# Optimization experiments

Hardware: AMD Instinct MI355X
Metric: run time of the kernel (lower is better)

The kernel has to match this reference:

```python
import math
import jax, jax.numpy as jnp
import numpy as np

H = 1024
NH = 16
HD = H // NH
FF = 4096


def gelu_erf(x):
    return x * 0.5 * (1.0 + jax.lax.erf(x / jnp.sqrt(jnp.float32(2.0))))


def layernorm(x, gamma, beta, eps=1e-12):
    mean = x.mean(axis=-1, keepdims=True)
    var = ((x - mean) ** 2).mean(axis=-1, keepdims=True)
    return gamma * (x - mean) / jnp.sqrt(var + eps) + beta


def setup_inputs() -> dict:
    key = jax.random.key(0)
    ks = jax.random.split(key, 12)
    B, S = 2, 2048
    sc = 0.02
    return {
        "x": jax.random.normal(ks[0], (B, S, H), jnp.float32),
        "attention_mask": jnp.ones((B, S), jnp.int32),
        "Wq": jax.random.normal(ks[1], (H, H), jnp.float32) * sc,
        "bq": jnp.zeros((H,), jnp.float32),
        "Wk": jax.random.normal(ks[2], (H, H), jnp.float32) * sc,
        "bk": jnp.zeros((H,), jnp.float32),
        "Wv": jax.random.normal(ks[3], (H, H), jnp.float32) * sc,
        "bv": jnp.zeros((H,), jnp.float32),
        "Wo": jax.random.normal(ks[4], (H, H), jnp.float32) * sc,
        "bo": jnp.zeros((H,), jnp.float32),
        "ln1_g": jnp.ones((H,), jnp.float32),
        "ln1_b": jnp.zeros((H,), jnp.float32),
        "W1": jax.random.normal(ks[5], (H, FF), jnp.float32) * sc,
        "b1": jnp.zeros((FF,), jnp.float32),
        "W2": jax.random.normal(ks[6], (FF, H), jnp.float32) * sc,
        "b2": jnp.zeros((H,), jnp.float32),
        "ln2_g": jnp.ones((H,), jnp.float32),
        "ln2_b": jnp.zeros((H,), jnp.float32),
    }


def reference(x, attention_mask, Wq, bq, Wk, bk, Wv, bv, Wo, bo,
              ln1_g, ln1_b, W1, b1, W2, b2, ln2_g, ln2_b):
    B, S, _ = x.shape
    # QKV projections, split heads -> [B, NH, S, HD]
    def split(t):
        return t.reshape(B, S, NH, HD).transpose(0, 2, 1, 3)
    q = split(x @ Wq + bq)
    k = split(x @ Wk + bk)
    v = split(x @ Wv + bv)
    # scores [B, NH, S, S]
    s = jnp.einsum("bhqd,bhkd->bhqk", q, k) / math.sqrt(HD)
    mask = (attention_mask == 1)[:, None, None, :]  # [B,1,1,S]
    s = jnp.where(mask, s, -jnp.inf)
    p = jax.nn.softmax(s, axis=-1)
    a = jnp.einsum("bhqk,bhkd->bhqd", p, v)
    a = a.transpose(0, 2, 1, 3).reshape(B, S, H)  # merge heads
    a = a @ Wo + bo
    a = layernorm(a, ln1_g, ln1_b)  # NOTE: no residual in source
    m = gelu_erf(a @ W1 + b1) @ W2 + b2
    return layernorm(m, ln2_g, ln2_b)
```

## Files before the change

### kernel.cpp

```cpp
#include <hip/hip_runtime.h>
#include <hip/hip_bf16.h>
#include <math.h>

typedef __bf16 bf16;
typedef __attribute__((ext_vector_type(8))) __bf16 bf16x8;
typedef __attribute__((ext_vector_type(4))) __bf16 bf16x4;
typedef __attribute__((ext_vector_type(4))) float f32x4;

#define HDIM 1024
#define NHEAD 16
#define HD 64
#define FFDIM 4096
#define BATCH 2
#define SEQ 2048
#define M_TOK 4096
#define PSTRIDE ((size_t)M_TOK * HDIM)

static __device__ __forceinline__ void async_load16(const bf16* g, bf16* l) {
  __builtin_amdgcn_global_load_lds(
      (const __attribute__((address_space(1))) void*)g,
      (__attribute__((address_space(3))) void*)l, 16, 0, 0);
}

__global__ __launch_bounds__(256)
void prep_kernel(const float* __restrict__ x,
                 const float* __restrict__ Wq, const float* __restrict__ Wk,
                 const float* __restrict__ Wv, const float* __restrict__ Wo,
                 const float* __restrict__ W1, const float* __restrict__ W2,
                 bf16* __restrict__ Xb, bf16* __restrict__ QKVT,
                 bf16* __restrict__ W1T, bf16* __restrict__ W2T)
{
  const int z = blockIdx.z;
  const int t = threadIdx.x;
  if (z == 12) {
    const size_t base = ((size_t)(blockIdx.y * 32 + blockIdx.x)) * 4096;
#pragma unroll
    for (int j = 0; j < 4; ++j) {
      const size_t i = base + j * 1024 + t * 4;
      f32x4 v = *(const f32x4*)(x + i);
      bf16x4 o;
#pragma unroll
      for (int k = 0; k < 4; ++k) o[k] = (bf16)v[k];
      *(bf16x4*)(Xb + i) = o;
    }
    return;
  }
  const float* ps; bf16* pd; int sld, dld;
  if (z < 4) {
    ps = (z == 0) ? Wq : (z == 1) ? Wk : (z == 2) ? Wv : Wo;
    pd = QKVT + (size_t)z * HDIM * HDIM; sld = 1024; dld = 1024;
  } else if (z < 8) {
    const int c = z - 4;
    ps = W1 + c * 1024; sld = 4096;
    pd = W1T + (size_t)c * 1024 * 1024; dld = 1024;
  } else {
    const int c = z - 8;
    ps = W2 + (size_t)c * 1024 * 1024; sld = 1024;
    pd = W2T + c * 1024; dld = 4096;
  }
  __shared__ float tile[32][33];
  const int tx = t & 31, ty = t >> 5;
  const int c0 = blockIdx.x * 32, r0 = blockIdx.y * 32;
#pragma unroll
  for (int i = 0; i < 32; i += 8)
    tile[ty + i][tx] = ps[(size_t)(r0 + ty + i) * sld + c0 + tx];
  __syncthreads();
#pragma unroll
  for (int i = 0; i < 32; i += 8)
    pd[(size_t)(c0 + ty + i) * dld + r0 + tx] = (bf16)tile[tx][ty + i];
}

template<int EPI>
__global__ __launch_bounds__(256)
void gemm_bt(const bf16* __restrict__ A, const bf16* __restrict__ Bt,
             const float* __restrict__ b0, const float* __restrict__ b1p,
             const float* __restrict__ b2p, void* __restrict__ Cout,
             int M, int N, int ldk, int kchunk)
{
  __shared__ __align__(16) bf16 As[128 * 64];
  __shared__ __align__(16) bf16 Bs[128 * 64];
  const int t = threadIdx.x;
  const int wave = t >> 6, lane = t & 63;
  const int lm = lane & 15, qd = lane >> 4;
  const int wm = (wave >> 1) * 64, wn = (wave & 1) * 64;
  const int bm = blockIdx.y * 128, bn = blockIdx.x * 128;
  const int kbeg = blockIdx.z * kchunk;

  f32x4 acc[4][4] = {};
  const int srow = t >> 3;
  const int schk = t & 7;

  for (int k0 = kbeg; k0 < kbeg + kchunk; k0 += 64) {
#pragma unroll
    for (int r = 0; r < 4; ++r) {
      const int row = r * 32 + srow;
      const int chunk = schk ^ (row & 7);
      async_load16(A + (size_t)(bm + row) * ldk + (k0 + chunk * 8),
                   (bf16*)((char*)As + r * 4096 + t * 16));
    }
#pragma unroll
    for (int r = 0; r < 4; ++r) {
      const int row = r * 32 + srow;
      const int chunk = schk ^ (row & 7);
      async_load16(Bt + (size_t)(bn + row) * ldk + (k0 + chunk * 8),
                   (bf16*)((char*)Bs + r * 4096 + t * 16));
    }
    __syncthreads();
#pragma unroll
    for (int ks = 0; ks < 2; ++ks) {
      bf16x8 av[4], bv[4];
#pragma unroll
      for (int mt = 0; mt < 4; ++mt) {
        const int row = wm + mt * 16 + lm;
        const int chunk = (ks * 4 + qd) ^ (row & 7);
        av[mt] = *(const bf16x8*)(As + row * 64 + chunk * 8);
      }
#pragma unroll
      for (int nt = 0; nt < 4; ++nt) {
        const int row = wn + nt * 16 + lm;
        const int chunk = (ks * 4 + qd) ^ (row & 7);
        bv[nt] = *(const bf16x8*)(Bs + row * 64 + chunk * 8);
      }
#pragma unroll
      for (int mt = 0; mt < 4; ++mt)
#pragma unroll
        for (int nt = 0; nt < 4; ++nt)
          acc[mt][nt] = __builtin_amdgcn_mfma_f32_16x16x32_bf16(av[mt], bv[nt], acc[mt][nt], 0, 0, 0);
    }
    __syncthreads();
  }

#pragma unroll
  for (int nt = 0; nt < 4; ++nt) {
    const int col = bn + wn + nt * 16 + lm;
    float bs = 0.f;
    if (EPI == 2) bs = b0[col];
    if (EPI == 3) {
      const int sect = col >> 10, c = col & 1023;
      bs = (sect == 0) ? b0[c] : (sect == 1) ? b1p[c] : b2p[c];
    }
#pragma unroll
    for (int mt = 0; mt < 4; ++mt) {
#pragma unroll
      for (int r = 0; r < 4; ++r) {
        const int row = bm + wm + mt * 16 + qd * 4 + r;
        float v = acc[mt][nt][r] + bs;
        if (EPI == 1) {
          ((float*)Cout + (size_t)blockIdx.z * M * N)[(size_t)row * N + col] = v;
        } else if (EPI == 2) {
          const float z = v * 0.70710678118f;
          const float az = fabsf(z);
          const float tt = __builtin_amdgcn_rcpf(fmaf(az, 0.3275911f, 1.0f));
          const float poly = tt * fmaf(tt, fmaf(tt, fmaf(tt, fmaf(tt, 1.061405429f,
                             -1.453152027f), 1.421413741f), -0.284496736f), 0.254829592f);
          const float e = __builtin_amdgcn_exp2f(az * az * -1.4426950408889634f);
          float erfv = 1.0f - poly * e;
          erfv = (z < 0.f) ? -erfv : erfv;
          const float g = 0.5f * v * (1.0f + erfv);
          ((bf16*)Cout)[(size_t)row * N + col] = (bf16)g;
        } else {
          bf16* base = (bf16*)Cout;
          const int sect = col >> 10, c = col & 1023;
          if (sect < 2) {
            base[(size_t)sect * M_TOK * HDIM + (size_t)row * HDIM + c] = (bf16)v;
          } else {
            const int hh = c >> 6, dd = c & 63;
            const int bb = row >> 11, ss = row & 2047;
            base[(size_t)2 * M_TOK * HDIM +
                 (size_t)((bb * NHEAD + hh) * HD + dd) * SEQ + ss] = (bf16)v;
          }
        }
      }
    }
  }
}

__global__ __launch_bounds__(256)
void attn_kernel(const bf16* __restrict__ Q, const bf16* __restrict__ Kg,
                 const bf16* __restrict__ Vt, const int* __restrict__ mask,
                 bf16* __restrict__ Aout)
{
  __shared__ __align__(16) bf16 Ks[64 * 64];
  __shared__ __align__(16) bf16 Vs[64 * 64];
  __shared__ __align__(16) bf16 Ps[4][16 * 64];
  __shared__ float madd[64];

  const int t = threadIdx.x;
  const int wave = t >> 6, lane = t & 63;
  const int lm = lane & 15, qd = lane >> 4;
  const int bh = blockIdx.y;
  const int b = bh >> 4, h = bh & 15;
  const int q0 = blockIdx.x * 64;
  const int qg = q0 + wave * 16 + lm;
  bf16* Psw = Ps[wave];

  bf16x8 qf[2];
#pragma unroll
  for (int ks = 0; ks < 2; ++ks)
    qf[ks] = *(const bf16x8*)(Q + (size_t)(b * SEQ + qg) * HDIM + h * HD + ks * 32 + qd * 8);

  float l_lane = 0.f;
  f32x4 oacc[4] = {};

  const int srow = t >> 3, schk = t & 7;
  const float C = 0.1803368801f;

  for (int kv0 = 0; kv0 < SEQ; kv0 += 64) {
#pragma unroll
    for (int r = 0; r < 2; ++r) {
      const int row = r * 32 + srow;
      const int g = schk ^ (row & 7);
      async_load16(Kg + (size_t)(b * SEQ + kv0 + row) * HDIM + h * HD + g * 8,
                   (bf16*)((char*)Ks + r * 4096 + t * 16));
      async_load16(Vt + (size_t)(bh * HD + row) * SEQ + kv0 + g * 8,
                   (bf16*)((char*)Vs + r * 4096 + t * 16));
    }
    if (t < 64) madd[t] = (mask[b * SEQ + kv0 + t] == 1) ? 0.f : -1.0e30f;
    __syncthreads();

    f32x4 sacc[4] = {};
#pragma unroll
    for (int ks = 0; ks < 2; ++ks) {
#pragma unroll
      for (int nt = 0; nt < 4; ++nt) {
        const int row = nt * 16 + lm;
        const int c = (ks * 4 + qd) ^ (row & 7);
        bf16x8 kf = *(const bf16x8*)(Ks + row * 64 + c * 8);
        sacc[nt] = __builtin_amdgcn_mfma_f32_16x16x32_bf16(kf, qf[ks], sacc[nt], 0, 0, 0);
      }
    }

#pragma unroll
    for (int nt = 0; nt < 4; ++nt) {
      f32x4 ma = *(const f32x4*)(madd + nt * 16 + qd * 4);
      bf16x4 pk;
#pragma unroll
      for (int r = 0; r < 4; ++r) {
        const float pv = __builtin_amdgcn_exp2f(fmaf(sacc[nt][r], C, ma[r]));
        l_lane += pv;
        pk[r] = (bf16)pv;
      }
      *(bf16x4*)((char*)Psw + lm * 128 +
                 (((nt * 2 + (qd >> 1)) ^ (lm & 7)) * 16) + (qd & 1) * 8) = pk;
    }

#pragma unroll
    for (int ks = 0; ks < 2; ++ks) {
      bf16x8 pf = *(const bf16x8*)((char*)Psw + lm * 128 + (((ks * 4 + qd) ^ (lm & 7)) * 16));
#pragma unroll
      for (int nt = 0; nt < 4; ++nt) {
        const int row = nt * 16 + lm;
        const int c = (ks * 4 + qd) ^ (row & 7);
        bf16x8 vf = *(const bf16x8*)(Vs + row * 64 + c * 8);
        oacc[nt] = __builtin_amdgcn_mfma_f32_16x16x32_bf16(vf, pf, oacc[nt], 0, 0, 0);
      }
    }
    __syncthreads();
  }

  float l = l_lane;
  l += __shfl_xor(l, 16, 64);
  l += __shfl_xor(l, 32, 64);
  const float inv = 1.0f / l;

#pragma unroll
  for (int nt = 0; nt < 4; ++nt) {
    bf16x4 ok;
#pragma unroll
    for (int r = 0; r < 4; ++r) ok[r] = (bf16)(oacc[nt][r] * inv);
    *(bf16x4*)((char*)Psw + lm * 128 +
               (((nt * 2 + (qd >> 1)) ^ (lm & 7)) * 16) + (qd & 1) * 8) = ok;
  }
#pragma unroll
  for (int rr = 0; rr < 2; ++rr) {
    const int ql = rr * 8 + (lane >> 3);
    const int cl = lane & 7;
    bf16x8 v = *(const bf16x8*)((char*)Psw + ql * 128 + ((cl ^ (ql & 7)) * 16));
    *(bf16x8*)(Aout + (size_t)(b * SEQ + q0 + wave * 16 + ql) * HDIM + h * HD + cl * 8) = v;
  }
}

template<int NP, int OUT_BF16>
__global__ __launch_bounds__(256)
void ln_sum(const float* __restrict__ p, const float* __restrict__ bias,
            const float* __restrict__ gamma, const float* __restrict__ beta,
            void* __restrict__ out)
{
  const int row = blockIdx.x;
  const int t = threadIdx.x;
  f32x4 v = *(const f32x4*)(p + (size_t)row * HDIM + t * 4);
#pragma unroll
  for (int np = 1; np < NP; ++np) {
    f32x4 u = *(const f32x4*)(p + np * PSTRIDE + (size_t)row * HDIM + t * 4);
#pragma unroll
    for (int j = 0; j < 4; ++j) v[j] += u[j];
  }
  f32x4 bv0 = *(const f32x4*)(bias + t * 4);
#pragma unroll
  for (int j = 0; j < 4; ++j) v[j] += bv0[j];

  float s = v[0] + v[1] + v[2] + v[3];
  float s2 = v[0] * v[0] + v[1] * v[1] + v[2] * v[2] + v[3] * v[3];
#pragma unroll
  for (int d = 1; d < 64; d <<= 1) { s += __shfl_xor(s, d, 64); s2 += __shfl_xor(s2, d, 64); }
  __shared__ float ss[4], ss2[4];
  const int wave = t >> 6, lane = t & 63;
  if (lane == 0) { ss[wave] = s; ss2[wave] = s2; }
  __syncthreads();
  s = ss[0] + ss[1] + ss[2] + ss[3];
  s2 = ss2[0] + ss2[1] + ss2[2] + ss2[3];
  const float mean = s * (1.0f / HDIM);
  const float var = s2 * (1.0f / HDIM) - mean * mean;
  const float rstd = rsqrtf(var + 1e-12f);
  f32x4 gv = *(const f32x4*)(gamma + t * 4);
  f32x4 bv = *(const f32x4*)(beta + t * 4);
  f32x4 y;
#pragma unroll
  for (int j = 0; j < 4; ++j) y[j] = gv[j] * (v[j] - mean) * rstd + bv[j];
  if (OUT_BF16) {
    bf16x4 o;
#pragma unroll
    for (int j = 0; j < 4; ++j) o[j] = (bf16)y[j];
    *(bf16x4*)((bf16*)out + (size_t)row * HDIM + t * 4) = o;
  } else {
    *(f32x4*)((float*)out + (size_t)row * HDIM + t * 4) = y;
  }
}

extern "C" void kernel_launch(void* const* d_in, const int* in_sizes, int n_in,
                              void* d_out, int out_size, void* d_ws, size_t ws_size,
                              hipStream_t stream)
{
  const float* x    = (const float*)d_in[0];
  const int*   am   = (const int*)d_in[1];
  const float* Wq   = (const float*)d_in[2];
  const float* bq   = (const float*)d_in[3];
  const float* Wk   = (const float*)d_in[4];
  const float* bk   = (const float*)d_in[5];
  const float* Wv   = (const float*)d_in[6];
  const float* bv   = (const float*)d_in[7];
  const float* Wo   = (const float*)d_in[8];
  const float* bo   = (const float*)d_in[9];
  const float* ln1g = (const float*)d_in[10];
  const float* ln1b = (const float*)d_in[11];
  const float* W1   = (const float*)d_in[12];
  const float* b1   = (const float*)d_in[13];
  const float* W2   = (const float*)d_in[14];
  const float* b2   = (const float*)d_in[15];
  const float* ln2g = (const float*)d_in[16];
  const float* ln2b = (const float*)d_in[17];

  char* ws = (char*)d_ws;
  const size_t MB = 1ull << 20;
  bf16*  W1T  = (bf16*)(ws + 0 * MB);
  bf16*  W2T  = (bf16*)(ws + 8 * MB);
  bf16*  Xb   = (bf16*)(ws + 16 * MB);
  bf16*  QKVT = (bf16*)(ws + 24 * MB);
  bf16*  WoT  = QKVT + (size_t)3 * HDIM * HDIM;
  bf16*  Qb   = (bf16*)(ws + 33 * MB);
  bf16*  Kb   = (bf16*)(ws + 41 * MB);
  bf16*  Vtb  = (bf16*)(ws + 49 * MB);
  bf16*  Ab   = (bf16*)(ws + 16 * MB);
  float* Pw   = (float*)(ws + 33 * MB);
  bf16*  L1   = (bf16*)(ws + 65 * MB);
  bf16*  F1   = (bf16*)(ws + 16 * MB);
  float* Pf   = (float*)(ws + 48 * MB);

  prep_kernel<<<dim3(32, 32, 13), 256, 0, stream>>>(x, Wq, Wk, Wv, Wo, W1, W2,
                                                    Xb, QKVT, W1T, W2T);

  gemm_bt<3><<<dim3(3072 / 128, M_TOK / 128, 1), 256, 0, stream>>>(
      Xb, QKVT, bq, bk, bv, Qb, M_TOK, 3072, HDIM, HDIM);

  attn_kernel<<<dim3(SEQ / 64, BATCH * NHEAD), 256, 0, stream>>>(Qb, Kb, Vtb, am, Ab);

  gemm_bt<1><<<dim3(HDIM / 128, M_TOK / 128, 2), 256, 0, stream>>>(
      Ab, WoT, nullptr, nullptr, nullptr, Pw, M_TOK, HDIM, HDIM, 512);
  ln_sum<2, 1><<<M_TOK, 256, 0, stream>>>(Pw, bo, ln1g, ln1b, L1);

  gemm_bt<2><<<dim3(FFDIM / 128, M_TOK / 128, 1), 256, 0, stream>>>(
      L1, W1T, b1, nullptr, nullptr, F1, M_TOK, FFDIM, HDIM, HDIM);

  if (ws_size >= 113 * MB) {
    gemm_bt<1><<<dim3(HDIM / 128, M_TOK / 128, 4), 256, 0, stream>>>(
        F1, W2T, nullptr, nullptr, nullptr, Pf, M_TOK, HDIM, FFDIM, 1024);
    ln_sum<4, 0><<<M_TOK, 256, 0, stream>>>(Pf, b2, ln2g, ln2b, (float*)d_out);
  } else {
    gemm_bt<1><<<dim3(HDIM / 128, M_TOK / 128, 2), 256, 0, stream>>>(
        F1, W2T, nullptr, nullptr, nullptr, Pf, M_TOK, HDIM, FFDIM, 2048);
    ln_sum<2, 0><<<M_TOK, 256, 0, stream>>>(Pf, b2, ln2g, ln2b, (float*)d_out);
  }
}
```

Before: 385.3 us.

## Split attention over KV halves with merge kernel and register-resident P

Splits the attention KV loop into two halves across a new grid dimension, so each block covers half the keys. Partial unnormalised outputs and row sums go to fp32 workspace, and a separate merge kernel sums them, normalises and writes bf16. The P tile now stays in registers and feeds 16x16x16 MFMAs directly instead of making a round trip through LDS. This adds fp32 partial traffic, an extra launch and smaller MFMA shapes in exchange for twice as many blocks and no LDS staging of P.

```diff
diff --git a/kernel.cpp b/kernel.cpp
--- a/kernel.cpp
+++ b/kernel.cpp
@@ -6,6 +6,7 @@
 typedef __attribute__((ext_vector_type(8))) __bf16 bf16x8;
 typedef __attribute__((ext_vector_type(4))) __bf16 bf16x4;
 typedef __attribute__((ext_vector_type(4))) float f32x4;
+typedef __attribute__((ext_vector_type(4))) short short4v;
 
 #define HDIM 1024
 #define NHEAD 16
@@ -14,12 +15,26 @@
 #define BATCH 2
 #define SEQ 2048
 #define M_TOK 4096
+#define NSPLIT 2
 #define PSTRIDE ((size_t)M_TOK * HDIM)
 
 static __device__ __forceinline__ void async_load16(const bf16* g, bf16* l) {
   __builtin_amdgcn_global_load_lds(
       (const __attribute__((address_space(1))) void*)g,
       (__attribute__((address_space(3))) void*)l, 16, 0, 0);
+}
+
+static __device__ __forceinline__ f32x4 mfma16_bf16(bf16x4 a, bf16x4 b, f32x4 c) {
+#if defined(__HIP_DEVICE_COMPILE__)
+#if __has_builtin(__builtin_amdgcn_mfma_f32_16x16x16bf16_1k)
+  return __builtin_amdgcn_mfma_f32_16x16x16bf16_1k(
+      __builtin_bit_cast(short4v, a), __builtin_bit_cast(short4v, b), c, 0, 0, 0);
+#else
+  return __builtin_amdgcn_mfma_f32_16x16x16_bf16(a, b, c, 0, 0, 0);
+#endif
+#else
+  return c;
+#endif
 }
 
 __global__ __launch_bounds__(256)
@@ -178,11 +193,10 @@
 __global__ __launch_bounds__(256)
 void attn_kernel(const bf16* __restrict__ Q, const bf16* __restrict__ Kg,
                  const bf16* __restrict__ Vt, const int* __restrict__ mask,
-                 bf16* __restrict__ Aout)
+                 float* __restrict__ Po, float* __restrict__ Lp)
 {
   __shared__ __align__(16) bf16 Ks[64 * 64];
   __shared__ __align__(16) bf16 Vs[64 * 64];
-  __shared__ __align__(16) bf16 Ps[4][16 * 64];
   __shared__ float madd[64];
 
   const int t = threadIdx.x;
@@ -192,7 +206,8 @@
   const int b = bh >> 4, h = bh & 15;
   const int q0 = blockIdx.x * 64;
   const int qg = q0 + wave * 16 + lm;
-  bf16* Psw = Ps[wave];
+  const int split = blockIdx.z;
+  const int kv_beg = split * (SEQ / NSPLIT);
 
   bf16x8 qf[2];
 #pragma unroll
@@ -205,7 +220,7 @@
   const int srow = t >> 3, schk = t & 7;
   const float C = 0.1803368801f;
 
-  for (int kv0 = 0; kv0 < SEQ; kv0 += 64) {
+  for (int kv0 = kv_beg; kv0 < kv_beg + SEQ / NSPLIT; kv0 += 64) {
 #pragma unroll
     for (int r = 0; r < 2; ++r) {
       const int row = r * 32 + srow;
@@ -230,29 +245,26 @@
       }
     }
 
+    bf16x4 pf4[4];
 #pragma unroll
     for (int nt = 0; nt < 4; ++nt) {
       f32x4 ma = *(const f32x4*)(madd + nt * 16 + qd * 4);
-      bf16x4 pk;
 #pragma unroll
       for (int r = 0; r < 4; ++r) {
         const float pv = __builtin_amdgcn_exp2f(fmaf(sacc[nt][r], C, ma[r]));
         l_lane += pv;
-        pk[r] = (bf16)pv;
-      }
-      *(bf16x4*)((char*)Psw + lm * 128 +
-                 (((nt * 2 + (qd >> 1)) ^ (lm & 7)) * 16) + (qd & 1) * 8) = pk;
-    }
-
-#pragma unroll
-    for (int ks = 0; ks < 2; ++ks) {
-      bf16x8 pf = *(const bf16x8*)((char*)Psw + lm * 128 + (((ks * 4 + qd) ^ (lm & 7)) * 16));
+        pf4[nt][r] = (bf16)pv;
+      }
+    }
+
+#pragma unroll
+    for (int nt2 = 0; nt2 < 4; ++nt2) {
+      const int row = nt2 * 16 + lm;
 #pragma unroll
       for (int nt = 0; nt < 4; ++nt) {
-        const int row = nt * 16 + lm;
-        const int c = (ks * 4 + qd) ^ (row & 7);
-        bf16x8 vf = *(const bf16x8*)(Vs + row * 64 + c * 8);
-        oacc[nt] = __builtin_amdgcn_mfma_f32_16x16x32_bf16(vf, pf, oacc[nt], 0, 0, 0);
+        bf16x4 vf = *(const bf16x4*)(Vs + row * 64 +
+                     (((nt * 2 + (qd >> 1)) ^ (row & 7)) * 8) + (qd & 1) * 4);
+        oacc[nt2] = mfma16_bf16(vf, pf4[nt], oacc[nt2]);
       }
     }
     __syncthreads();
@@ -261,23 +273,45 @@
   float l = l_lane;
   l += __shfl_xor(l, 16, 64);
   l += __shfl_xor(l, 32, 64);
+
+  float* po = Po + ((size_t)(split * 32 + bh) * 64) * SEQ;
+#pragma unroll
+  for (int nt2 = 0; nt2 < 4; ++nt2)
+#pragma unroll
+    for (int r = 0; r < 4; ++r)
+      po[(size_t)(nt2 * 16 + qd * 4 + r) * SEQ + q0 + wave * 16 + lm] = oacc[nt2][r];
+  if (qd == 0)
+    Lp[(size_t)(split * 32 + bh) * SEQ + q0 + wave * 16 + lm] = l;
+}
+
+__global__ __launch_bounds__(256)
+void attn_merge(const float* __restrict__ Po, const float* __restrict__ Lp,
+                bf16* __restrict__ Aout)
+{
+  const int t = threadIdx.x;
+  const int bh = blockIdx.y;
+  const int b = bh >> 4, h = bh & 15;
+  const int s0 = blockIdx.x * 64;
+  const int tok = t >> 2;
+  const int dc = (t & 3) * 16;
+
+  const float l = Lp[(size_t)bh * SEQ + s0 + tok] +
+                  Lp[(size_t)(32 + bh) * SEQ + s0 + tok];
   const float inv = 1.0f / l;
 
-#pragma unroll
-  for (int nt = 0; nt < 4; ++nt) {
-    bf16x4 ok;
-#pragma unroll
-    for (int r = 0; r < 4; ++r) ok[r] = (bf16)(oacc[nt][r] * inv);
-    *(bf16x4*)((char*)Psw + lm * 128 +
-               (((nt * 2 + (qd >> 1)) ^ (lm & 7)) * 16) + (qd & 1) * 8) = ok;
-  }
-#pragma unroll
-  for (int rr = 0; rr < 2; ++rr) {
-    const int ql = rr * 8 + (lane >> 3);
-    const int cl = lane & 7;
-    bf16x8 v = *(const bf16x8*)((char*)Psw + ql * 128 + ((cl ^ (ql & 7)) * 16));
-    *(bf16x8*)(Aout + (size_t)(b * SEQ + q0 + wave * 16 + ql) * HDIM + h * HD + cl * 8) = v;
-  }
+  const float* p0 = Po + ((size_t)bh * 64) * SEQ + s0 + tok;
+  const float* p1 = Po + ((size_t)(32 + bh) * 64) * SEQ + s0 + tok;
+  bf16x8 o0, o1;
+#pragma unroll
+  for (int j = 0; j < 8; ++j)
+    o0[j] = (bf16)((p0[(size_t)(dc + j) * SEQ] + p1[(size_t)(dc + j) * SEQ]) * inv);
+#pragma unroll
+  for (int j = 8; j < 16; ++j)
+    o1[j - 8] = (bf16)((p0[(size_t)(dc + j) * SEQ] + p1[(size_t)(dc + j) * SEQ]) * inv);
+
+  bf16* dst = Aout + (size_t)(b * SEQ + s0 + tok) * HDIM + h * HD + dc;
+  *(bf16x8*)dst = o0;
+  *(bf16x8*)(dst + 8) = o1;
 }
 
 template<int NP, int OUT_BF16>
@@ -360,6 +394,8 @@
   bf16*  Qb   = (bf16*)(ws + 33 * MB);
   bf16*  Kb   = (bf16*)(ws + 41 * MB);
   bf16*  Vtb  = (bf16*)(ws + 49 * MB);
+  float* Po   = (float*)(ws + 57 * MB);
+  float* Lp   = (float*)(ws + 89 * MB);
   bf16*  Ab   = (bf16*)(ws + 16 * MB);
   float* Pw   = (float*)(ws + 33 * MB);
   bf16*  L1   = (bf16*)(ws + 65 * MB);
@@ -372,7 +408,9 @@
   gemm_bt<3><<<dim3(3072 / 128, M_TOK / 128, 1), 256, 0, stream>>>(
       Xb, QKVT, bq, bk, bv, Qb, M_TOK, 3072, HDIM, HDIM);
 
-  attn_kernel<<<dim3(SEQ / 64, BATCH * NHEAD), 256, 0, stream>>>(Qb, Kb, Vtb, am, Ab);
+  attn_kernel<<<dim3(SEQ / 64, BATCH * NHEAD, NSPLIT), 256, 0, stream>>>(
+      Qb, Kb, Vtb, am, Po, Lp);
+  attn_merge<<<dim3(SEQ / 64, BATCH * NHEAD), 256, 0, stream>>>(Po, Lp, Ab);
 
   gemm_bt<1><<<dim3(HDIM / 128, M_TOK / 128, 2), 256, 0, stream>>>(
       Ab, WoT, nullptr, nullptr, nullptr, Pw, M_TOK, HDIM, HDIM, 512);
```

After: 387.0 us. Within noise of the previous version (+0.4%).
